# Performance work log

Measured on AMD Instinct MI355X. Metric: run time of the kernel, lower is better.

The kernel has to match this reference:

```python
import jax, jax.numpy as jnp
import numpy as np

DIM = 1024
MLP_DIM = 4096
EPS = 1e-5


def layer_norm(x, gamma, beta):
    mean = jnp.mean(x, axis=-1, keepdims=True)
    var = jnp.mean(jnp.square(x - mean), axis=-1, keepdims=True)  # unbiased=False
    return gamma * (x - mean) / jnp.sqrt(var + EPS) + beta


def setup_inputs() -> dict:
    key = jax.random.key(0)
    ks = jax.random.split(key, 12)
    s = 0.02
    return {
        "x": jax.random.normal(ks[0], (4, 2048, DIM), dtype=jnp.float32),
        "gamma1": jnp.ones((DIM,), jnp.float32),
        "beta1": jnp.zeros((DIM,), jnp.float32),
        "gamma2": jnp.ones((DIM,), jnp.float32),
        "beta2": jnp.zeros((DIM,), jnp.float32),
        "Wq": jax.random.normal(ks[1], (DIM, DIM), jnp.float32) * s,
        "bq": jnp.zeros((DIM,), jnp.float32),
        "Wk": jax.random.normal(ks[2], (DIM, DIM), jnp.float32) * s,
        "bk": jnp.zeros((DIM,), jnp.float32),
        "Wv": jax.random.normal(ks[3], (DIM, DIM), jnp.float32) * s,
        "bv": jnp.zeros((DIM,), jnp.float32),
        "W1": jax.random.normal(ks[4], (DIM, MLP_DIM), jnp.float32) * s,
        "b1": jnp.zeros((MLP_DIM,), jnp.float32),
        "W2": jax.random.normal(ks[5], (MLP_DIM, DIM), jnp.float32) * s,
        "b2": jnp.zeros((DIM,), jnp.float32),
    }


def reference(x, gamma1, beta1, gamma2, beta2, Wq, bq, Wk, bk, Wv, bv, W1, b1, W2, b2):
    # Pre-LN attention sub-block (single-head manual attention over full dim)
    residual = x
    h = layer_norm(x, gamma1, beta1)
    q = h @ Wq + bq  # [B,S,D]
    k = h @ Wk + bk
    v = h @ Wv + bv
    scale = 1.0 / jnp.sqrt(jnp.asarray(q.shape[-1], q.dtype))
    scores = jnp.einsum("bsd,btd->bst", q, k) * scale  # [B,S,S]
    attn = jax.nn.softmax(scores, axis=-1)
    x = jnp.einsum("bst,btd->bsd", attn, v) + residual
    # Pre-LN MLP sub-block
    residual = x
    h = layer_norm(x, gamma2, beta2)
    h = jax.nn.gelu(h @ W1 + b1, approximate=False)  # torch F.gelu exact
    x = h @ W2 + b2 + residual
    return x
```

## Files before the change

kernel.cpp:

```cpp
#include <hip/hip_runtime.h>
#include <hip/hip_bf16.h>
#include <math.h>

typedef __bf16 bf16x8 __attribute__((ext_vector_type(8)));
typedef float  f32x4  __attribute__((ext_vector_type(4)));
typedef __hip_bfloat16 bf16;

#define DIM  1024
#define MLPD 4096
#define NB   4
#define SEQ  2048
#define ROWS (NB * SEQ)

__device__ __forceinline__ void gload_lds16(const void* g, void* l) {
  __builtin_amdgcn_global_load_lds(
      (__attribute__((address_space(1))) void*)(g),
      (__attribute__((address_space(3))) void*)(l), 16, 0, 0);
}

__device__ __forceinline__ void bar() {
  asm volatile("" ::: "memory");
  __builtin_amdgcn_s_barrier();
  asm volatile("" ::: "memory");
}

template <int N>
__device__ __forceinline__ void vmw() {
  asm volatile("s_waitcnt vmcnt(%0)" ::"n"(N) : "memory");
}

__device__ __forceinline__ bf16 to_bf16(float v) { return __float2bfloat16(v); }
__device__ __forceinline__ bf16 to_bf16(bf16 v)  { return v; }

__device__ __forceinline__ float gelu_exact_fast(float v) {
  const float x  = v * 0.70710678118654752f;
  const float ax = fabsf(x);
  const float t  = __builtin_amdgcn_rcpf(1.0f + 0.3275911f * ax);
  const float p  = t * (0.254829592f +
                   t * (-0.284496736f +
                   t * (1.421413741f +
                   t * (-1.453152027f + t * 1.061405429f))));
  float erf = 1.0f - p * __expf(-x * x);
  erf = copysignf(erf, x);
  return 0.5f * v * (1.0f + erf);
}

template <int EPI>
__global__ __launch_bounds__(512, 2) void gemm256(
    const bf16* __restrict__ A,  long aBatch, int lda,
    const bf16* __restrict__ Bt, long bBatch, int ldb,
    void* __restrict__ Cout,     long cBatch, int ldc,
    const float* __restrict__ bias, int K, float scale)
{
  extern __shared__ char smem[];

  const int gx = gridDim.x, gy = gridDim.y;
  int flat = blockIdx.x + gx * (blockIdx.y + gy * blockIdx.z);
  const int nwg = gx * gy * gridDim.z;
  flat = (flat & 7) * (nwg >> 3) + (flat >> 3);
  const int bx = flat % gx;
  const int t2 = flat / gx;
  const int by = t2 % gy;
  const int bz = t2 / gy;

  const long rowBase = (long)by * 256;
  const long colBase = (long)bx * 256;
  const long ldaB = (long)lda * 2, ldbB = (long)ldb * 2;
  const char* Ag = (const char*)(A + bz * aBatch + rowBase * lda);
  const char* Bg = (const char*)(Bt + bz * bBatch + colBase * ldb);

  const int tid  = threadIdx.x;
  const int lane = tid & 63;
  const int wave = tid >> 6;
  const int wm = wave >> 2, wn = wave & 3;
  const int fr = lane & 15, fq = lane >> 4;
  const int fh2 = fr >> 1;
  const int sA = (((fr & 1) << 2) | fq) ^ fh2;
  const int rdCom = fh2 * 128 + sA * 16;

  long offA[2], offB[2];
#pragma unroll
  for (int li = 0; li < 2; ++li) {
    const int d = li * 512 + tid;
    {
      const int wms = d >> 9, kks = (d >> 8) & 1, w = d & 255;
      const int pr = w >> 3, s = w & 7, u = s ^ (pr & 7);
      offA[li] = (long)(wms * 128 + pr * 2 + (u >> 2)) * ldaB +
                 kks * 64 + (u & 3) * 16;
    }
    {
      const int wns = d >> 8, kkb = (d >> 7) & 1, w = d & 127;
      const int pr = w >> 3, s = w & 7, u = s ^ (pr & 7);
      offB[li] = (long)(wns * 64 + pr * 2 + (u >> 2)) * ldbB +
                 kkb * 64 + (u & 3) * 16;
    }
  }
  const int dstOff = tid * 16;
  const long aHalf = ldaB << 6;
  const long bHalf = ldbB << 5;

  const int NT = K >> 6;

  bf16x8 a[4][2], b[2][2][2];
  f32x4 acc[8][4] = {};

#define STG_A(J, mh)                                                           \
  do {                                                                         \
    char* _d = smem + (((J) & 1) << 16) + (mh) * 16384 + dstOff;               \
    const char* _s = Ag + (J) * 128 + (mh) * aHalf;                            \
    gload_lds16(_s + offA[0], _d);                                             \
    gload_lds16(_s + offA[1], _d + 8192);                                      \
  } while (0)

#define STG_B(J, nh)                                                           \
  do {                                                                         \
    char* _d = smem + (((J) & 1) << 16) + 32768 + (nh) * 16384 + dstOff;       \
    const char* _s = Bg + (J) * 128 + (nh) * bHalf;                            \
    gload_lds16(_s + offB[0], _d);                                             \
    gload_lds16(_s + offB[1], _d + 8192);                                      \
  } while (0)

#define LDA(mh, J)                                                             \
  do {                                                                         \
    const char* _b = smem + (((J) & 1) << 16) + (mh) * 16384 + wm * 8192 +     \
                     rdCom;                                                    \
    _Pragma("unroll") for (int m = 0; m < 4; ++m)                              \
      _Pragma("unroll") for (int kk = 0; kk < 2; ++kk)                         \
        a[m][kk] = *(const bf16x8*)(_b + kk * 4096 + m * 1024);                \
  } while (0)

#define LDB(nh, J)                                                             \
  do {                                                                         \
    const char* _b = smem + (((J) & 1) << 16) + 32768 + (nh) * 16384 +         \
                     wn * 4096 + rdCom;                                        \
    _Pragma("unroll") for (int n = 0; n < 2; ++n)                              \
      _Pragma("unroll") for (int kk = 0; kk < 2; ++kk)                         \
        b[nh][n][kk] = *(const bf16x8*)(_b + kk * 2048 + n * 1024);            \
  } while (0)

#define MM(mh, nh)                                                             \
  do {                                                                         \
    __builtin_amdgcn_s_setprio(1);                                             \
    _Pragma("unroll") for (int m = 0; m < 4; ++m)                              \
      _Pragma("unroll") for (int n = 0; n < 2; ++n)                            \
        _Pragma("unroll") for (int kk = 0; kk < 2; ++kk)                       \
          acc[(mh) * 4 + m][(nh) * 2 + n] =                                    \
              __builtin_amdgcn_mfma_f32_16x16x32_bf16(                         \
                  a[m][kk], b[nh][n][kk], acc[(mh) * 4 + m][(nh) * 2 + n],     \
                  0, 0, 0);                                                    \
    __builtin_amdgcn_s_setprio(0);                                             \
  } while (0)

#define LGKM0 asm volatile("s_waitcnt lgkmcnt(0)" ::: "memory")

#define TILE(J, S1, S2, VN)                                                    \
  do {                                                                         \
    LDA(0, J); LDB(0, J);                                                      \
    if (S1) STG_A((J) + 1, 1);                                                 \
    bar(); LGKM0; MM(0, 0); bar();                                             \
    LDB(1, J);                                                                 \
    if (S2) STG_A((J) + 2, 0);                                                 \
    bar(); LGKM0; MM(0, 1); bar();                                             \
    LDA(1, J);                                                                 \
    if (S2) STG_B((J) + 2, 0);                                                 \
    bar(); LGKM0; MM(1, 1); bar();                                             \
    if (S2) STG_B((J) + 2, 1);                                                 \
    vmw<VN>(); bar(); MM(1, 0); bar();                                         \
  } while (0)

  STG_A(0, 0); STG_B(0, 0); STG_B(0, 1); STG_A(0, 1);
  STG_A(1, 0); STG_B(1, 0); STG_B(1, 1);
  vmw<6>(); bar();

  for (int j = 0; j < NT - 2; ++j) TILE(j, true, true, 6);
  TILE(NT - 2, true, false, 0);
  TILE(NT - 1, false, false, 63);

#undef STG_A
#undef STG_B
#undef LDA
#undef LDB
#undef MM
#undef TILE

#pragma unroll
  for (int mh = 0; mh < 2; ++mh)
#pragma unroll
    for (int m = 0; m < 4; ++m)
#pragma unroll
      for (int nh = 0; nh < 2; ++nh)
#pragma unroll
        for (int n = 0; n < 2; ++n) {
          const long col = colBase + wn * 64 + nh * 32 + n * 16 + fr;
#pragma unroll
          for (int e = 0; e < 4; ++e) {
            const long r = rowBase + wm * 128 + mh * 64 + m * 16 + fq * 4 + e;
            float v = acc[mh * 4 + m][nh * 2 + n][e];
            if constexpr (EPI == 0) {
              v += bias[col];
              ((bf16*)Cout)[bz * cBatch + r * ldc + col] = __float2bfloat16(v);
            } else if constexpr (EPI == 3) {
              v += bias[col];
              ((bf16*)Cout)[bz * cBatch + r * ldc + col] =
                  __float2bfloat16(gelu_exact_fast(v));
            } else {
              ((bf16*)Cout)[bz * cBatch + r * ldc + col] =
                  __float2bfloat16(v * scale);
            }
          }
        }
}

template <int EPI>
__global__ __launch_bounds__(256, 4) void gemm128(
    const bf16* __restrict__ A,  long aBatch, int lda,
    const bf16* __restrict__ Bt, long bBatch, int ldb,
    void* __restrict__ Cout,     long cBatch, int ldc,
    const float* __restrict__ bias,
    const float* __restrict__ resid, long rBatch, int ldr,
    int K, float scale)
{
  __shared__ char smem[2][16384];

  const int gx = gridDim.x, gy = gridDim.y;
  const int n = gx * gy * gridDim.z;
  const int f = blockIdx.x + gx * (blockIdx.y + gy * blockIdx.z);
  const int o = (f & 7) * (n >> 3) + (f >> 3);
  const int sx = gx >> 3;
  int st = o >> 6;
  const int w = o & 63;
  const int spz = sx * (gy >> 3);
  const int bz = st / spz; st -= bz * spz;
  const int sty = st / sx, stx = st - sty * sx;
  const int by = sty * 8 + (w >> 3), bx = stx * 8 + (w & 7);

  const long rowBase = (long)by * 128;
  const long colBase = (long)bx * 128;
  const long ldaB = (long)lda * 2, ldbB = (long)ldb * 2;
  const char* Ag = (const char*)(A + bz * aBatch + rowBase * lda);
  const char* Bg = (const char*)(Bt + bz * bBatch + colBase * ldb);

  const int tid  = threadIdx.x;
  const int lane = tid & 63;
  const int wave = tid >> 6;
  const int wm = wave >> 1, wn = wave & 1;
  const int fr = lane & 15, fq = lane >> 4;

  const int fh = fr >> 1;
  const int sA = (((fr & 1) << 2) | fq) ^ fh;
  const int laneRd = fh * 128 + sA * 16;
  const int abase = wm * 4096 + laneRd;
  const int bbase = 8192 + wn * 4096 + laneRd;

  const int t0   = wave * 128 + lane;
  const int r2   = t0 >> 3;
  const int u0   = (t0 & 7) ^ (r2 & 7);
  const int row0 = r2 * 2 + (u0 >> 2);
  const int kc0  = u0 & 3;
  const char* aSrc0 = Ag + (long)row0 * ldaB + kc0 * 16;
  const char* aSrc1 = aSrc0 + 16 * ldaB;
  const char* bSrc0 = Bg + (long)row0 * ldbB + kc0 * 16;
  const char* bSrc1 = bSrc0 + 16 * ldbB;
  const int doff = wave * 2048 + lane * 16;

  const int NT = K >> 5;
  f32x4 acc[4][4] = {};

#define STAGE(WB)                                                              \
  do {                                                                         \
    gload_lds16(aSrc0, &smem[WB][doff]);                                       \
    gload_lds16(aSrc1, &smem[WB][doff + 1024]);                                \
    gload_lds16(bSrc0, &smem[WB][8192 + doff]);                                \
    gload_lds16(bSrc1, &smem[WB][8192 + doff + 1024]);                         \
    aSrc0 += 64; aSrc1 += 64; bSrc0 += 64; bSrc1 += 64;                        \
  } while (0)

#define READMM(RB)                                                             \
  do {                                                                         \
    const char* _r = &smem[RB][0];                                             \
    bf16x8 av[4], bv[4];                                                       \
    _Pragma("unroll") for (int m = 0; m < 4; ++m)                              \
      av[m] = *(const bf16x8*)(_r + abase + m * 1024);                         \
    _Pragma("unroll") for (int nn = 0; nn < 4; ++nn)                           \
      bv[nn] = *(const bf16x8*)(_r + bbase + nn * 1024);                       \
    __builtin_amdgcn_s_setprio(1);                                             \
    _Pragma("unroll") for (int m = 0; m < 4; ++m)                              \
      _Pragma("unroll") for (int nn = 0; nn < 4; ++nn)                         \
        acc[m][nn] = __builtin_amdgcn_mfma_f32_16x16x32_bf16(                  \
            av[m], bv[nn], acc[m][nn], 0, 0, 0);                               \
    __builtin_amdgcn_s_setprio(0);                                             \
  } while (0)

  for (int t = 0; t < NT; t += 2) {
    STAGE(0);
    STAGE(1);
    vmw<0>(); bar();
    READMM(0);
    READMM(1);
    bar();
  }

#undef STAGE
#undef READMM

#pragma unroll
  for (int m = 0; m < 4; ++m) {
#pragma unroll
    for (int nn = 0; nn < 4; ++nn) {
      const long col = colBase + wn * 64 + nn * 16 + fr;
#pragma unroll
      for (int e = 0; e < 4; ++e) {
        const long r = rowBase + wm * 64 + m * 16 + fq * 4 + e;
        float v = acc[m][nn][e];
        if constexpr (EPI == 2) {
          v += resid[bz * rBatch + r * ldr + col];
          ((float*)Cout)[bz * cBatch + r * ldc + col] = v;
        } else if constexpr (EPI == 3) {
          v += bias[col];
          ((bf16*)Cout)[bz * cBatch + r * ldc + col] =
              __float2bfloat16(gelu_exact_fast(v));
        } else {
          v += bias[col] + resid[r * (long)ldr + col];
          ((float*)Cout)[bz * cBatch + r * ldc + col] = v;
        }
      }
    }
  }
}

__global__ __launch_bounds__(256) void ln_kernel(
    const float* __restrict__ x, const float* __restrict__ gamma,
    const float* __restrict__ beta, bf16* __restrict__ out)
{
  const long row = blockIdx.x;
  const float4 v = ((const float4*)(x + row * DIM))[threadIdx.x];
  float s  = v.x + v.y + v.z + v.w;
  float ss = v.x * v.x + v.y * v.y + v.z * v.z + v.w * v.w;
  const int lane = threadIdx.x & 63, wave = threadIdx.x >> 6;
#pragma unroll
  for (int o = 32; o; o >>= 1) { s += __shfl_xor(s, o); ss += __shfl_xor(ss, o); }
  __shared__ float rs[4], rss[4];
  if (lane == 0) { rs[wave] = s; rss[wave] = ss; }
  __syncthreads();
  s  = rs[0] + rs[1] + rs[2] + rs[3];
  ss = rss[0] + rss[1] + rss[2] + rss[3];
  const float mean = s * (1.0f / DIM);
  const float var  = ss * (1.0f / DIM) - mean * mean;
  const float rstd = rsqrtf(var + 1e-5f);
  const float4 g = ((const float4*)gamma)[threadIdx.x];
  const float4 b = ((const float4*)beta)[threadIdx.x];
  union { bf16 h[4]; uint2 u; } pk;
  pk.h[0] = __float2bfloat16(g.x * (v.x - mean) * rstd + b.x);
  pk.h[1] = __float2bfloat16(g.y * (v.y - mean) * rstd + b.y);
  pk.h[2] = __float2bfloat16(g.z * (v.z - mean) * rstd + b.z);
  pk.h[3] = __float2bfloat16(g.w * (v.w - mean) * rstd + b.w);
  ((uint2*)(out + row * DIM))[threadIdx.x] = pk.u;
}

__global__ __launch_bounds__(256) void softmax_kernel(bf16* __restrict__ scores)
{
  const long row = blockIdx.x;
  bf16* rp = scores + row * (long)SEQ;
  union { bf16 h[8]; uint4 u; } in;
  in.u = ((const uint4*)rp)[threadIdx.x];
  float f[8];
#pragma unroll
  for (int j = 0; j < 8; ++j) f[j] = __bfloat162float(in.h[j]);
  const int lane = threadIdx.x & 63, wave = threadIdx.x >> 6;
  float mx = f[0];
#pragma unroll
  for (int j = 1; j < 8; ++j) mx = fmaxf(mx, f[j]);
#pragma unroll
  for (int o = 32; o; o >>= 1) mx = fmaxf(mx, __shfl_xor(mx, o));
  __shared__ float rm[4], rsum[4];
  if (lane == 0) rm[wave] = mx;
  __syncthreads();
  mx = fmaxf(fmaxf(rm[0], rm[1]), fmaxf(rm[2], rm[3]));
  float sum = 0.0f;
#pragma unroll
  for (int j = 0; j < 8; ++j) { f[j] = expf(f[j] - mx); sum += f[j]; }
#pragma unroll
  for (int o = 32; o; o >>= 1) sum += __shfl_xor(sum, o);
  if (lane == 0) rsum[wave] = sum;
  __syncthreads();
  sum = rsum[0] + rsum[1] + rsum[2] + rsum[3];
  const float inv = 1.0f / sum;
  union { bf16 h[8]; uint4 u; } pk;
#pragma unroll
  for (int j = 0; j < 8; ++j) pk.h[j] = __float2bfloat16(f[j] * inv);
  ((uint4*)rp)[threadIdx.x] = pk.u;
}

template <typename TI>
__global__ __launch_bounds__(256) void transpose_bf16_kernel(
    const TI* __restrict__ in, bf16* __restrict__ out,
    int ldIn, int ldOut, long inBatch, long outBatch)
{
  __shared__ bf16 tile[32][33];
  const long zin  = (long)blockIdx.z * inBatch;
  const long zout = (long)blockIdx.z * outBatch;
  const int c0 = blockIdx.x * 32, r0 = blockIdx.y * 32;
  const int tx = threadIdx.x & 31, ty = threadIdx.x >> 5;
#pragma unroll
  for (int i = 0; i < 32; i += 8)
    tile[ty + i][tx] = to_bf16(in[zin + (long)(r0 + ty + i) * ldIn + c0 + tx]);
  __syncthreads();
#pragma unroll
  for (int i = 0; i < 32; i += 8)
    out[zout + (long)(c0 + ty + i) * ldOut + r0 + tx] = tile[tx][ty + i];
}

__global__ __launch_bounds__(256) void concat3_kernel(
    const float* __restrict__ a, const float* __restrict__ b,
    const float* __restrict__ c, float* __restrict__ o)
{
  const int i = blockIdx.x * 256 + threadIdx.x;
  if (i < DIM) { o[i] = a[i]; o[DIM + i] = b[i]; o[2 * DIM + i] = c[i]; }
}

extern "C" void kernel_launch(void* const* d_in, const int* in_sizes, int n_in,
                              void* d_out, int out_size, void* d_ws, size_t ws_size,
                              hipStream_t stream) {
  const float* x   = (const float*)d_in[0];
  const float* g1  = (const float*)d_in[1];
  const float* be1 = (const float*)d_in[2];
  const float* g2  = (const float*)d_in[3];
  const float* be2 = (const float*)d_in[4];
  const float* Wq  = (const float*)d_in[5];
  const float* bq  = (const float*)d_in[6];
  const float* Wk  = (const float*)d_in[7];
  const float* bk  = (const float*)d_in[8];
  const float* Wv  = (const float*)d_in[9];
  const float* bv  = (const float*)d_in[10];
  const float* W1  = (const float*)d_in[11];
  const float* b1  = (const float*)d_in[12];
  const float* W2  = (const float*)d_in[13];
  const float* b2  = (const float*)d_in[14];
  float* out = (float*)d_out;

  char* ws = (char*)d_ws;
  bf16* WqkvT = (bf16*)(ws + 0);
  bf16* W1T   = (bf16*)(ws + (6l << 20));
  bf16* W2T   = (bf16*)(ws + (14l << 20));
  float* bqkv = (float*)(ws + (22l << 20));
  bf16* h     = (bf16*)(ws + (23l << 20));
  bf16* qkv   = (bf16*)(ws + (39l << 20));
  bf16* vT    = (bf16*)(ws + (87l << 20));
  bf16* sc    = (bf16*)(ws + (103l << 20));
  bf16* g_act = (bf16*)sc;

  const int SMEM = 131072;
  hipFuncSetAttribute(reinterpret_cast<const void*>(&gemm256<0>),
                      hipFuncAttributeMaxDynamicSharedMemorySize, SMEM);
  hipFuncSetAttribute(reinterpret_cast<const void*>(&gemm256<5>),
                      hipFuncAttributeMaxDynamicSharedMemorySize, SMEM);

  const dim3 blk(256), gblk(512);

  concat3_kernel<<<4, blk, 0, stream>>>(bq, bk, bv, bqkv);
  transpose_bf16_kernel<float><<<dim3(32, 32, 1), blk, 0, stream>>>(
      Wq, WqkvT, DIM, DIM, 0, 0);
  transpose_bf16_kernel<float><<<dim3(32, 32, 1), blk, 0, stream>>>(
      Wk, WqkvT + (long)DIM * DIM, DIM, DIM, 0, 0);
  transpose_bf16_kernel<float><<<dim3(32, 32, 1), blk, 0, stream>>>(
      Wv, WqkvT + 2l * DIM * DIM, DIM, DIM, 0, 0);
  transpose_bf16_kernel<float><<<dim3(128, 32, 1), blk, 0, stream>>>(
      W1, W1T, MLPD, DIM, 0, 0);
  transpose_bf16_kernel<float><<<dim3(32, 128, 1), blk, 0, stream>>>(
      W2, W2T, DIM, MLPD, 0, 0);

  ln_kernel<<<ROWS, blk, 0, stream>>>(x, g1, be1, h);

  gemm256<0><<<dim3(12, 32, 1), gblk, SMEM, stream>>>(
      h, 0, DIM, WqkvT, 0, DIM, qkv, 0, 3 * DIM, bqkv, DIM, 1.0f);

  transpose_bf16_kernel<bf16><<<dim3(32, 64, NB), blk, 0, stream>>>(
      qkv + 2 * DIM, vT, 3 * DIM, SEQ, (long)SEQ * 3 * DIM, (long)DIM * SEQ);

  gemm256<5><<<dim3(8, 8, NB), gblk, SMEM, stream>>>(
      qkv, (long)SEQ * 3 * DIM, 3 * DIM, qkv + DIM, (long)SEQ * 3 * DIM,
      3 * DIM, sc, (long)SEQ * SEQ, SEQ, nullptr, DIM, 0.03125f);

  softmax_kernel<<<ROWS, blk, 0, stream>>>(sc);

  gemm128<2><<<dim3(8, 16, NB), blk, 0, stream>>>(
      sc, (long)SEQ * SEQ, SEQ, vT, (long)DIM * SEQ, SEQ,
      out, (long)SEQ * DIM, DIM, nullptr, x, (long)SEQ * DIM, DIM, SEQ, 1.0f);

  ln_kernel<<<ROWS, blk, 0, stream>>>(out, g2, be2, h);

  gemm128<3><<<dim3(32, 64, 1), blk, 0, stream>>>(
      h, 0, DIM, W1T, 0, DIM, g_act, 0, MLPD, b1, nullptr, 0, 0, DIM, 1.0f);

  gemm128<4><<<dim3(8, 64, 1), blk, 0, stream>>>(
      g_act, 0, MLPD, W2T, 0, MLPD, out, 0, DIM, b2, out, 0, DIM, MLPD, 1.0f);
}
```

Before: 373.7 us.

## Add 128x64 GEMM tile for narrow-N GEMMs and fuse weight prep kernels

Adds a gemm64 kernel with 128x64 output tiles and uses it for the attention-times-V GEMM and the W2 down-projection. Both have N=1024, so the smaller tile doubles the block count and should fill the CUs better. Also merges the five weight transposes and the bias concat into one prep kernel to cut launch overhead. The cost is less operand reuse per tile, meaning more global/LDS traffic per FLOP; the epilogue branches are also reshuffled between the gemm variants.

```diff
diff --git a/kernel.cpp b/kernel.cpp
--- a/kernel.cpp
+++ b/kernel.cpp
@@ -199,10 +199,6 @@
             if constexpr (EPI == 0) {
               v += bias[col];
               ((bf16*)Cout)[bz * cBatch + r * ldc + col] = __float2bfloat16(v);
-            } else if constexpr (EPI == 3) {
-              v += bias[col];
-              ((bf16*)Cout)[bz * cBatch + r * ldc + col] =
-                  __float2bfloat16(gelu_exact_fast(v));
             } else {
               ((bf16*)Cout)[bz * cBatch + r * ldc + col] =
                   __float2bfloat16(v * scale);
@@ -312,13 +308,127 @@
       for (int e = 0; e < 4; ++e) {
         const long r = rowBase + wm * 64 + m * 16 + fq * 4 + e;
         float v = acc[m][nn][e];
+        if constexpr (EPI == 3) {
+          v += bias[col];
+          ((bf16*)Cout)[bz * cBatch + r * ldc + col] =
+              __float2bfloat16(gelu_exact_fast(v));
+        } else {
+          v += bias[col] + resid[r * (long)ldr + col];
+          ((float*)Cout)[bz * cBatch + r * ldc + col] = v;
+        }
+      }
+    }
+  }
+}
+
+template <int EPI>
+__global__ __launch_bounds__(256, 4) void gemm64(
+    const bf16* __restrict__ A,  long aBatch, int lda,
+    const bf16* __restrict__ Bt, long bBatch, int ldb,
+    void* __restrict__ Cout,     long cBatch, int ldc,
+    const float* __restrict__ bias,
+    const float* __restrict__ resid, long rBatch, int ldr,
+    int K, float scale)
+{
+  __shared__ char smem[2][12288];
+
+  const int gx = gridDim.x, gy = gridDim.y;
+  const int n = gx * gy * gridDim.z;
+  const int f = blockIdx.x + gx * (blockIdx.y + gy * blockIdx.z);
+  const int o = (f & 7) * (n >> 3) + (f >> 3);
+  const int sx = gx >> 3;
+  int st = o >> 6;
+  const int w = o & 63;
+  const int spz = sx * (gy >> 3);
+  const int bz = st / spz; st -= bz * spz;
+  const int sty = st / sx, stx = st - sty * sx;
+  const int by = sty * 8 + (w >> 3), bx = stx * 8 + (w & 7);
+
+  const long rowBase = (long)by * 128;
+  const long colBase = (long)bx * 64;
+  const long ldaB = (long)lda * 2, ldbB = (long)ldb * 2;
+  const char* Ag = (const char*)(A + bz * aBatch + rowBase * lda);
+  const char* Bg = (const char*)(Bt + bz * bBatch + colBase * ldb);
+
+  const int tid  = threadIdx.x;
+  const int lane = tid & 63;
+  const int wave = tid >> 6;
+  const int wm = wave >> 1, wn = wave & 1;
+  const int fr = lane & 15, fq = lane >> 4;
+
+  const int fh = fr >> 1;
+  const int sA = (((fr & 1) << 2) | fq) ^ fh;
+  const int laneRd = fh * 128 + sA * 16;
+  const int abase = wm * 4096 + laneRd;
+  const int bbase = 8192 + wn * 2048 + laneRd;
+
+  const char* aSrcA[2];
+#pragma unroll
+  for (int li = 0; li < 2; ++li) {
+    const int t = li * 256 + tid;
+    const int r2 = t >> 3;
+    const int u  = (t & 7) ^ (r2 & 7);
+    aSrcA[li] = Ag + (long)(r2 * 2 + (u >> 2)) * ldaB + (u & 3) * 16;
+  }
+  const int r2b = tid >> 3;
+  const int ub  = (tid & 7) ^ (r2b & 7);
+  const char* bSrcP = Bg + (long)(r2b * 2 + (ub >> 2)) * ldbB + (ub & 3) * 16;
+  const int dA0 = tid * 16, dA1 = 4096 + tid * 16, dB = 8192 + tid * 16;
+
+  const int NT = K >> 5;
+  f32x4 acc[4][2] = {};
+  const char* a0 = aSrcA[0];
+  const char* a1 = aSrcA[1];
+  const char* b0 = bSrcP;
+
+#define STAGE(WB)                                                              \
+  do {                                                                         \
+    gload_lds16(a0, &smem[WB][dA0]);                                           \
+    gload_lds16(a1, &smem[WB][dA1]);                                           \
+    gload_lds16(b0, &smem[WB][dB]);                                            \
+    a0 += 64; a1 += 64; b0 += 64;                                              \
+  } while (0)
+
+#define READMM(RB)                                                             \
+  do {                                                                         \
+    const char* _r = &smem[RB][0];                                             \
+    bf16x8 av[4], bv[2];                                                       \
+    _Pragma("unroll") for (int m = 0; m < 4; ++m)                              \
+      av[m] = *(const bf16x8*)(_r + abase + m * 1024);                         \
+    _Pragma("unroll") for (int nn = 0; nn < 2; ++nn)                           \
+      bv[nn] = *(const bf16x8*)(_r + bbase + nn * 1024);                       \
+    __builtin_amdgcn_s_setprio(1);                                             \
+    _Pragma("unroll") for (int m = 0; m < 4; ++m)                              \
+      _Pragma("unroll") for (int nn = 0; nn < 2; ++nn)                         \
+        acc[m][nn] = __builtin_amdgcn_mfma_f32_16x16x32_bf16(                  \
+            av[m], bv[nn], acc[m][nn], 0, 0, 0);                               \
+    __builtin_amdgcn_s_setprio(0);                                             \
+  } while (0)
+
+  for (int t = 0; t < NT; t += 2) {
+    STAGE(0);
+    STAGE(1);
+    vmw<0>(); bar();
+    READMM(0);
+    READMM(1);
+    bar();
+  }
+
+#undef STAGE
+#undef READMM
+
+#pragma unroll
+  for (int m = 0; m < 4; ++m) {
+#pragma unroll
+    for (int nn = 0; nn < 2; ++nn) {
+      const long col = colBase + wn * 32 + nn * 16 + fr;
+#pragma unroll
+      for (int e = 0; e < 4; ++e) {
+        const long r = rowBase + wm * 64 + m * 16 + fq * 4 + e;
+        float v = acc[m][nn][e];
         if constexpr (EPI == 2) {
           v += resid[bz * rBatch + r * ldr + col];
           ((float*)Cout)[bz * cBatch + r * ldc + col] = v;
-        } else if constexpr (EPI == 3) {
-          v += bias[col];
-          ((bf16*)Cout)[bz * cBatch + r * ldc + col] =
-              __float2bfloat16(gelu_exact_fast(v));
         } else {
           v += bias[col] + resid[r * (long)ldr + col];
           ((float*)Cout)[bz * cBatch + r * ldc + col] = v;
@@ -391,9 +501,8 @@
   ((uint4*)rp)[threadIdx.x] = pk.u;
 }
 
-template <typename TI>
-__global__ __launch_bounds__(256) void transpose_bf16_kernel(
-    const TI* __restrict__ in, bf16* __restrict__ out,
+__global__ __launch_bounds__(256) void transpose_v_kernel(
+    const bf16* __restrict__ in, bf16* __restrict__ out,
     int ldIn, int ldOut, long inBatch, long outBatch)
 {
   __shared__ bf16 tile[32][33];
@@ -403,19 +512,50 @@
   const int tx = threadIdx.x & 31, ty = threadIdx.x >> 5;
 #pragma unroll
   for (int i = 0; i < 32; i += 8)
-    tile[ty + i][tx] = to_bf16(in[zin + (long)(r0 + ty + i) * ldIn + c0 + tx]);
+    tile[ty + i][tx] = in[zin + (long)(r0 + ty + i) * ldIn + c0 + tx];
   __syncthreads();
 #pragma unroll
   for (int i = 0; i < 32; i += 8)
     out[zout + (long)(c0 + ty + i) * ldOut + r0 + tx] = tile[tx][ty + i];
 }
 
-__global__ __launch_bounds__(256) void concat3_kernel(
-    const float* __restrict__ a, const float* __restrict__ b,
-    const float* __restrict__ c, float* __restrict__ o)
+__global__ __launch_bounds__(256) void prep_kernel(
+    const float* __restrict__ Wq, const float* __restrict__ Wk,
+    const float* __restrict__ Wv, const float* __restrict__ W1,
+    const float* __restrict__ W2,
+    const float* __restrict__ bq, const float* __restrict__ bk,
+    const float* __restrict__ bv,
+    bf16* __restrict__ WqkvT, bf16* __restrict__ W1T,
+    bf16* __restrict__ W2T, float* __restrict__ bqkv)
 {
-  const int i = blockIdx.x * 256 + threadIdx.x;
-  if (i < DIM) { o[i] = a[i]; o[DIM + i] = b[i]; o[2 * DIM + i] = c[i]; }
+  int l = blockIdx.x;
+  if (l >= 11264) {
+    const int i = (l - 11264) * 256 + threadIdx.x;
+    bqkv[i] = bq[i]; bqkv[DIM + i] = bk[i]; bqkv[2 * DIM + i] = bv[i];
+    return;
+  }
+  __shared__ bf16 tile[32][33];
+  const float* in; bf16* out; int ldIn, ldOut, gxw;
+  if (l < 3072) {
+    const int wsel = l / 1024;
+    in = (wsel == 0) ? Wq : (wsel == 1) ? Wk : Wv;
+    out = WqkvT + (long)wsel * DIM * DIM;
+    l &= 1023; ldIn = DIM; ldOut = DIM; gxw = 32;
+  } else if (l < 7168) {
+    in = W1; out = W1T; l -= 3072; ldIn = MLPD; ldOut = DIM; gxw = 128;
+  } else {
+    in = W2; out = W2T; l -= 7168; ldIn = DIM; ldOut = MLPD; gxw = 32;
+  }
+  const int bxx = l % gxw, byy = l / gxw;
+  const int c0 = bxx * 32, r0 = byy * 32;
+  const int tx = threadIdx.x & 31, ty = threadIdx.x >> 5;
+#pragma unroll
+  for (int i = 0; i < 32; i += 8)
+    tile[ty + i][tx] = __float2bfloat16(in[(long)(r0 + ty + i) * ldIn + c0 + tx]);
+  __syncthreads();
+#pragma unroll
+  for (int i = 0; i < 32; i += 8)
+    out[(long)(c0 + ty + i) * ldOut + r0 + tx] = tile[tx][ty + i];
 }
 
 extern "C" void kernel_launch(void* const* d_in, const int* in_sizes, int n_in,
@@ -457,24 +597,15 @@
 
   const dim3 blk(256), gblk(512);
 
-  concat3_kernel<<<4, blk, 0, stream>>>(bq, bk, bv, bqkv);
-  transpose_bf16_kernel<float><<<dim3(32, 32, 1), blk, 0, stream>>>(
-      Wq, WqkvT, DIM, DIM, 0, 0);
-  transpose_bf16_kernel<float><<<dim3(32, 32, 1), blk, 0, stream>>>(
-      Wk, WqkvT + (long)DIM * DIM, DIM, DIM, 0, 0);
-  transpose_bf16_kernel<float><<<dim3(32, 32, 1), blk, 0, stream>>>(
-      Wv, WqkvT + 2l * DIM * DIM, DIM, DIM, 0, 0);
-  transpose_bf16_kernel<float><<<dim3(128, 32, 1), blk, 0, stream>>>(
-      W1, W1T, MLPD, DIM, 0, 0);
-  transpose_bf16_kernel<float><<<dim3(32, 128, 1), blk, 0, stream>>>(
-      W2, W2T, DIM, MLPD, 0, 0);
+  prep_kernel<<<11268, blk, 0, stream>>>(Wq, Wk, Wv, W1, W2, bq, bk, bv,
+                                         WqkvT, W1T, W2T, bqkv);
 
   ln_kernel<<<ROWS, blk, 0, stream>>>(x, g1, be1, h);
 
   gemm256<0><<<dim3(12, 32, 1), gblk, SMEM, stream>>>(
       h, 0, DIM, WqkvT, 0, DIM, qkv, 0, 3 * DIM, bqkv, DIM, 1.0f);
 
-  transpose_bf16_kernel<bf16><<<dim3(32, 64, NB), blk, 0, stream>>>(
+  transpose_v_kernel<<<dim3(32, 64, NB), blk, 0, stream>>>(
       qkv + 2 * DIM, vT, 3 * DIM, SEQ, (long)SEQ * 3 * DIM, (long)DIM * SEQ);
 
   gemm256<5><<<dim3(8, 8, NB), gblk, SMEM, stream>>>(
@@ -483,7 +614,7 @@
 
   softmax_kernel<<<ROWS, blk, 0, stream>>>(sc);
 
-  gemm128<2><<<dim3(8, 16, NB), blk, 0, stream>>>(
+  gemm64<2><<<dim3(16, 16, NB), blk, 0, stream>>>(
       sc, (long)SEQ * SEQ, SEQ, vT, (long)DIM * SEQ, SEQ,
       out, (long)SEQ * DIM, DIM, nullptr, x, (long)SEQ * DIM, DIM, SEQ, 1.0f);
 
@@ -492,6 +623,6 @@
   gemm128<3><<<dim3(32, 64, 1), blk, 0, stream>>>(
       h, 0, DIM, W1T, 0, DIM, g_act, 0, MLPD, b1, nullptr, 0, 0, DIM, 1.0f);
 
-  gemm128<4><<<dim3(8, 64, 1), blk, 0, stream>>>(
+  gemm64<4><<<dim3(16, 64, 1), blk, 0, stream>>>(
       g_act, 0, MLPD, W2T, 0, MLPD, out, 0, DIM, b2, out, 0, DIM, MLPD, 1.0f);
 }
```

Result: slower. 385.6 us (+3.2%).
